# Kernel optimization log

Measured on AMD Instinct MI355X. Metric: run time of the kernel, lower is better.

Reference implementation:

```python
import jax, jax.numpy as jnp
import numpy as np
from functools import partial

INPUT_DIM = 256
HIDDEN = 512
NUM_LAYERS = 2

def _linp(key, fan_in, shape):
    # torch nn.Linear/Conv default init: U(-1/sqrt(fan_in), 1/sqrt(fan_in))
    bound = 1.0 / np.sqrt(fan_in)
    return jax.random.uniform(key, shape, jnp.float32, -bound, bound)

def setup_inputs() -> dict:
    key = jax.random.key(0)
    ks = iter(jax.random.split(key, 64))
    d = {}
    d["x"] = jax.random.normal(next(ks), (32, 16, 1, 64, 64), jnp.float32)
    # encoder convs (OIHW)
    d["conv1_w"] = _linp(next(ks), 1 * 9, (16, 1, 3, 3));   d["conv1_b"] = _linp(next(ks), 1 * 9, (16,))
    d["conv2_w"] = _linp(next(ks), 16 * 9, (32, 16, 3, 3)); d["conv2_b"] = _linp(next(ks), 16 * 9, (32,))
    d["conv3_w"] = _linp(next(ks), 32 * 9, (INPUT_DIM, 32, 3, 3)); d["conv3_b"] = _linp(next(ks), 32 * 9, (INPUT_DIM,))
    # LSTM cells: per layer 4 gate linears (forget, input, cell, output), in = input+hidden
    for j in range(NUM_LAYERS):
        fan = (INPUT_DIM if j == 0 else HIDDEN) + HIDDEN
        for g in ("f", "i", "g", "o"):
            d[f"W{g}{j}"] = _linp(next(ks), fan, (fan, HIDDEN))
            d[f"b{g}{j}"] = _linp(next(ks), fan, (HIDDEN,))
    # classifier
    d["cw1"] = _linp(next(ks), HIDDEN, (HIDDEN, 128)); d["cb1"] = _linp(next(ks), HIDDEN, (128,))
    d["cw2"] = _linp(next(ks), 128, (128, 64));        d["cb2"] = _linp(next(ks), 128, (64,))
    d["cw3"] = _linp(next(ks), 64, (64, 6));           d["cb3"] = _linp(next(ks), 64, (6,))
    return d

def _conv(x, w, b):
    y = jax.lax.conv_general_dilated(x, w, (1, 1), "SAME",
                                     dimension_numbers=("NCHW", "OIHW", "NCHW"))
    return y + b[None, :, None, None]

def _maxpool2(x):
    return jax.lax.reduce_window(x, -jnp.inf, jax.lax.max,
                                 (1, 1, 2, 2), (1, 1, 2, 2), "VALID")

def reference(x, conv1_w, conv1_b, conv2_w, conv2_b, conv3_w, conv3_b,
              Wf0, bf0, Wi0, bi0, Wg0, bg0, Wo0, bo0,
              Wf1, bf1, Wi1, bi1, Wg1, bg1, Wo1, bo1,
              cw1, cb1, cw2, cb2, cw3, cb3):
    B, T, C, H, W = x.shape
    xf = x.reshape(B * T, C, H, W)
    h = _maxpool2(jax.nn.relu(_conv(xf, conv1_w, conv1_b)))
    h = _maxpool2(jax.nn.relu(_conv(h, conv2_w, conv2_b)))
    h = jax.nn.relu(_conv(h, conv3_w, conv3_b))
    emb = h.mean(axis=(2, 3)).reshape(B, T, -1)  # AdaptiveAvgPool2d((1,1)); dropout = identity (eval)

    layers = [(Wf0, bf0, Wi0, bi0, Wg0, bg0, Wo0, bo0),
              (Wf1, bf1, Wi1, bi1, Wg1, bg1, Wo1, bo1)]

    def step(carry, x_t):
        hs, cs = carry
        inp = x_t
        new_h, new_c = [], []
        for j, (Wf, bf, Wi, bi, Wg, bg, Wo, bo) in enumerate(layers):
            comb = jnp.concatenate([inp, hs[j]], axis=1)  # [B, in+H]
            f_t = jax.nn.sigmoid(comb @ Wf + bf)
            i_t = jax.nn.sigmoid(comb @ Wi + bi)
            g_t = jnp.tanh(comb @ Wg + bg)
            o_t = jax.nn.sigmoid(comb @ Wo + bo)
            c_n = f_t * cs[j] + i_t * g_t
            h_n = o_t * jnp.tanh(c_n)
            new_h.append(h_n); new_c.append(c_n)
            inp = h_n
        return (tuple(new_h), tuple(new_c)), None

    h0 = tuple(jnp.zeros((B, HIDDEN), x.dtype) for _ in range(NUM_LAYERS))
    c0 = tuple(jnp.zeros((B, HIDDEN), x.dtype) for _ in range(NUM_LAYERS))
    (hs, _), _ = jax.lax.scan(step, (h0, c0), jnp.swapaxes(emb, 0, 1))
    last = hs[-1]  # [B, HIDDEN], last timestep top-layer h (dropout = identity)

    y = jax.nn.relu(last @ cw1 + cb1)
    y = jax.nn.relu(y @ cw2 + cb2)
    return y @ cw3 + cb3  # [B, 6]
```

## Files before the change

kernel.cpp:

```cpp
#include <hip/hip_runtime.h>
#include <math.h>

__global__ void k_conv1(const float* __restrict__ x, const float* __restrict__ w,
                        const float* __restrict__ bias, float* __restrict__ out) {
  int idx = blockIdx.x * 256 + threadIdx.x;
  int ox = idx & 31, oy = (idx >> 5) & 31, oc = (idx >> 10) & 15, n = idx >> 14;
  const float* im = x + n * 4096;
  float wv[9];
#pragma unroll
  for (int i = 0; i < 9; ++i) wv[i] = w[oc * 9 + i];
  float bs = bias[oc];
  float m = 0.f;
#pragma unroll
  for (int dy = 0; dy < 2; ++dy)
#pragma unroll
    for (int dx = 0; dx < 2; ++dx) {
      int cy = oy * 2 + dy, cx = ox * 2 + dx;
      float s = bs;
#pragma unroll
      for (int ky = 0; ky < 3; ++ky) {
        int yy = cy + ky - 1;
        if (yy < 0 || yy >= 64) continue;
#pragma unroll
        for (int kx = 0; kx < 3; ++kx) {
          int xx = cx + kx - 1;
          if (xx < 0 || xx >= 64) continue;
          s += im[yy * 64 + xx] * wv[ky * 3 + kx];
        }
      }
      m = fmaxf(m, fmaxf(s, 0.f));
    }
  out[idx] = m;
}

__global__ void k_prep_w(const float* __restrict__ w2, float* __restrict__ w2t,
                         const float* __restrict__ w3, float* __restrict__ w3t) {
  int id = blockIdx.x * 256 + threadIdx.x;
  if (id < 73728) {
    int ct = id >> 8, oc = id & 255;
    int c = ct / 9, tap = ct - 9 * c;
    w3t[id] = w3[(oc * 32 + c) * 9 + tap];
  }
  if (id < 4608) {
    int ct = id >> 5, oc = id & 31;
    int c = ct / 9, tap = ct - 9 * c;
    w2t[id] = w2[(oc * 16 + c) * 9 + tap];
  }
}

__global__ __launch_bounds__(256) void k_conv2(
    const float* __restrict__ a1, const float* __restrict__ w2t,
    const float* __restrict__ bias, float* __restrict__ a2) {
  __shared__ __align__(16) float ins[8 * 1024];
  int n = blockIdx.x, ocg = blockIdx.y;
  int tid = threadIdx.x;
  int py = tid >> 4, px = tid & 15;
  int y0 = 2 * py - 1, x0 = 2 * px - 1;
  float acc[16][4] = {};
  const float* wb = w2t + ocg * 16;
  for (int ph = 0; ph < 2; ++ph) {
    __syncthreads();
    const float4* src = (const float4*)(a1 + n * 16384 + ph * 8192);
    for (int i = tid; i < 2048; i += 256) ((float4*)ins)[i] = src[i];
    __syncthreads();
    for (int c = 0; c < 8; ++c) {
      float wv[4][4];
#pragma unroll
      for (int r = 0; r < 4; ++r) {
        int y = y0 + r;
        bool vy = (y >= 0) && (y < 32);
        int yc = vy ? y : 0;
#pragma unroll
        for (int cc = 0; cc < 4; ++cc) {
          int xx = x0 + cc;
          bool vx = (xx >= 0) && (xx < 32);
          int xc = vx ? xx : 0;
          float t = ins[c * 1024 + yc * 32 + xc];
          wv[r][cc] = (vy && vx) ? t : 0.f;
        }
      }
      int ch = ph * 8 + c;
#pragma unroll
      for (int ky = 0; ky < 3; ++ky)
#pragma unroll
        for (int kx = 0; kx < 3; ++kx) {
          const float* w16 = wb + (ch * 9 + ky * 3 + kx) * 32;
#pragma unroll
          for (int i = 0; i < 4; ++i) {
            float vv = wv[(i >> 1) + ky][(i & 1) + kx];
#pragma unroll
            for (int j = 0; j < 16; ++j) acc[j][i] += vv * w16[j];
          }
        }
    }
  }
  const float* bp = bias + ocg * 16;
  float4 o[4];
#pragma unroll
  for (int j = 0; j < 16; ++j) {
    float m = fmaxf(fmaxf(acc[j][0], acc[j][1]), fmaxf(acc[j][2], acc[j][3]));
    ((float*)o)[j] = fmaxf(m + bp[j], 0.f);
  }
  float4* dst = (float4*)(a2 + (size_t)(n * 256 + tid) * 32 + ocg * 16);
#pragma unroll
  for (int q = 0; q < 4; ++q) dst[q] = o[q];
}

__global__ __launch_bounds__(256) void k_conv3(
    const float* __restrict__ a2, const float* __restrict__ w3t,
    const float* __restrict__ bias, float* __restrict__ comb0) {
  __shared__ __align__(16) float ins[324 * 20];
  int n = blockIdx.x, ocb = blockIdx.y;
  int tid = threadIdx.x;
  for (int i = tid; i < 1620; i += 256) ((float4*)ins)[i] = float4{0.f, 0.f, 0.f, 0.f};
  int wvid = __builtin_amdgcn_readfirstlane(tid >> 6);
  int lane = tid & 63;
  int tr = lane >> 4, tc = lane & 15;
  float acc[4][8] = {};
  const float* wbase = w3t + ocb * 32 + wvid * 8;
  const float4* src = (const float4*)(a2 + (size_t)n * 8192);
  for (int hf = 0; hf < 2; ++hf) {
    __syncthreads();
    for (int i = tid; i < 1024; i += 256) {
      int px = i >> 2, cg = i & 3;
      int p = ((px >> 4) + 1) * 18 + (px & 15) + 1;
      ((float4*)ins)[p * 5 + cg] = src[px * 8 + hf * 4 + cg];
    }
    __syncthreads();
    for (int cg = 0; cg < 4; ++cg) {
      float4 v[6][3];
#pragma unroll
      for (int dr = 0; dr < 6; ++dr)
#pragma unroll
        for (int dc = 0; dc < 3; ++dc)
          v[dr][dc] = ((const float4*)ins)[((4 * tr + dr) * 18 + tc + dc) * 5 + cg];
#pragma unroll
      for (int ky = 0; ky < 3; ++ky)
#pragma unroll
        for (int kx = 0; kx < 3; ++kx)
#pragma unroll
          for (int c = 0; c < 4; ++c) {
            const float* w8 = wbase + (((hf * 4 + cg) * 4 + c) * 9 + ky * 3 + kx) * 256;
#pragma unroll
            for (int i = 0; i < 4; ++i) {
              float vv = ((const float*)&v[i + ky][kx])[c];
#pragma unroll
              for (int j = 0; j < 8; ++j) acc[i][j] += vv * w8[j];
            }
          }
    }
  }
  const float* bp = bias + ocb * 32 + wvid * 8;
  int bb = n >> 4, tt = n & 15;
#pragma unroll
  for (int j = 0; j < 8; ++j) {
    float bj = bp[j];
    float s = 0.f;
#pragma unroll
    for (int i = 0; i < 4; ++i) s += fmaxf(acc[i][j] + bj, 0.f);
#pragma unroll
    for (int off = 32; off; off >>= 1) s += __shfl_down(s, off, 64);
    if (lane == 0) {
      int oc = ocb * 32 + wvid * 8 + j;
      comb0[(size_t)(tt * 768 + oc) * 32 + bb] = s * (1.f / 256.f);
    }
  }
}

__global__ void k_pack(const float* __restrict__ Wf, const float* __restrict__ Wi,
                       const float* __restrict__ Wg, const float* __restrict__ Wo,
                       float* __restrict__ p, int fan) {
  __shared__ float t[4][32][33];
  int k0 = blockIdx.x * 32, h0 = blockIdx.y * 32;
  int tx = threadIdx.x & 31, ty = threadIdx.x >> 5;
  const float* Ws[4] = {Wf, Wi, Wg, Wo};
#pragma unroll
  for (int g = 0; g < 4; ++g)
    for (int r = 0; r < 32; r += 8)
      t[g][ty + r][tx] = Ws[g][(size_t)(k0 + ty + r) * 512 + h0 + tx];
  __syncthreads();
  for (int r = 0; r < 32; r += 8) {
    int hh = ty + r;
    float4 v = {t[0][tx][hh], t[1][tx][hh], t[2][tx][hh], t[3][tx][hh]};
    ((float4*)p)[(size_t)(h0 + hh) * fan + k0 + tx] = v;
  }
}

struct SArgs {
  const float* comb;
  const float* pw;
  float* houtA; float* houtB; float* cT;
  const float* bf; const float* bi; const float* bg; const float* bo;
};

template <int FAN>
__device__ __forceinline__ void lstm_sbody(int h, int tid, const SArgs& A,
                                           float* __restrict__ gsum) {
  constexpr int CH = FAN / 8;
  const int wv = __builtin_amdgcn_readfirstlane(tid >> 6);
  const int lane = tid & 63;
  const int ks = lane >> 5, b = lane & 31;
  const int kb = wv * CH;
  const float4* pw4 = (const float4*)A.pw + (size_t)h * FAN + kb;
  const float* ac = A.comb + (size_t)kb * 32 + lane;
  float a0 = 0.f, a1 = 0.f, a2 = 0.f, a3 = 0.f;
#pragma unroll 8
  for (int kk = 0; kk < CH; kk += 2) {
    float4 w0 = pw4[kk];
    float4 w1 = pw4[kk + 1];
    float av = ac[kk * 32];
    a0 += av * (ks ? w1.x : w0.x);
    a1 += av * (ks ? w1.y : w0.y);
    a2 += av * (ks ? w1.z : w0.z);
    a3 += av * (ks ? w1.w : w0.w);
  }
  a0 += __shfl_xor(a0, 32);
  a1 += __shfl_xor(a1, 32);
  a2 += __shfl_xor(a2, 32);
  a3 += __shfl_xor(a3, 32);
  if (lane < 32) {
    gsum[(wv * 4 + 0) * 33 + b] = a0;
    gsum[(wv * 4 + 1) * 33 + b] = a1;
    gsum[(wv * 4 + 2) * 33 + b] = a2;
    gsum[(wv * 4 + 3) * 33 + b] = a3;
  }
  __syncthreads();
  if (tid < 32) {
    float fp = A.bf[h], ip = A.bi[h], gp = A.bg[h], op = A.bo[h];
#pragma unroll
    for (int q = 0; q < 8; ++q) {
      fp += gsum[(q * 4 + 0) * 33 + tid];
      ip += gsum[(q * 4 + 1) * 33 + tid];
      gp += gsum[(q * 4 + 2) * 33 + tid];
      op += gsum[(q * 4 + 3) * 33 + tid];
    }
    float ft = 1.f / (1.f + expf(-fp));
    float it_ = 1.f / (1.f + expf(-ip));
    float gt = tanhf(gp);
    float ot = 1.f / (1.f + expf(-op));
    float cn = ft * A.cT[h * 32 + tid] + it_ * gt;
    A.cT[h * 32 + tid] = cn;
    float hn = ot * tanhf(cn);
    A.houtA[h * 32 + tid] = hn;
    A.houtB[h * 32 + tid] = hn;
  }
}

__global__ __launch_bounds__(512) void k_lstm_s0(SArgs a) {
  __shared__ float gsum[32 * 33];
  lstm_sbody<768>(blockIdx.x, threadIdx.x, a, gsum);
}
__global__ __launch_bounds__(512) void k_lstm_s1(SArgs a) {
  __shared__ float gsum[32 * 33];
  lstm_sbody<1024>(blockIdx.x, threadIdx.x, a, gsum);
}
__global__ __launch_bounds__(512) void k_lstm_spair(SArgs a0, SArgs a1) {
  __shared__ float gsum[32 * 33];
  if (blockIdx.x < 512)
    lstm_sbody<768>(blockIdx.x, threadIdx.x, a0, gsum);
  else
    lstm_sbody<1024>(blockIdx.x - 512, threadIdx.x, a1, gsum);
}

__global__ void k_cls(const float* __restrict__ h1T, const float* __restrict__ cw1,
                      const float* __restrict__ cb1, const float* __restrict__ cw2,
                      const float* __restrict__ cb2, const float* __restrict__ cw3,
                      const float* __restrict__ cb3, float* __restrict__ out) {
  __shared__ float hv[512];
  __shared__ float y1[128];
  __shared__ float y2[64];
  int b = blockIdx.x, tid = threadIdx.x;
  for (int i = tid; i < 512; i += 128) hv[i] = h1T[i * 32 + b];
  __syncthreads();
  float s = cb1[tid];
  for (int k = 0; k < 512; ++k) s += hv[k] * cw1[k * 128 + tid];
  y1[tid] = fmaxf(s, 0.f);
  __syncthreads();
  if (tid < 64) {
    float s2 = cb2[tid];
    for (int k = 0; k < 128; ++k) s2 += y1[k] * cw2[k * 64 + tid];
    y2[tid] = fmaxf(s2, 0.f);
  }
  __syncthreads();
  if (tid < 6) {
    float s3 = cb3[tid];
    for (int k = 0; k < 64; ++k) s3 += y2[k] * cw3[k * 6 + tid];
    out[b * 6 + tid] = s3;
  }
}

extern "C" void kernel_launch(void* const* d_in, const int* in_sizes, int n_in,
                              void* d_out, int out_size, void* d_ws, size_t ws_size,
                              hipStream_t stream) {
  const float* x  = (const float*)d_in[0];
  const float* w1 = (const float*)d_in[1];
  const float* b1 = (const float*)d_in[2];
  const float* w2 = (const float*)d_in[3];
  const float* b2 = (const float*)d_in[4];
  const float* w3 = (const float*)d_in[5];
  const float* b3 = (const float*)d_in[6];
  const float* cw1 = (const float*)d_in[23];
  const float* cb1 = (const float*)d_in[24];
  const float* cw2 = (const float*)d_in[25];
  const float* cb2 = (const float*)d_in[26];
  const float* cw3 = (const float*)d_in[27];
  const float* cb3 = (const float*)d_in[28];

  float* ws = (float*)d_ws;
  float* a1    = ws;
  float* p0    = ws;
  float* p1    = ws + 1572864;
  float* comb0 = ws + 3670016;
  float* comb1 = ws + 4087808;
  float* c0    = ws + 4644864;
  float* c1    = ws + 4661248;
  float* a2    = ws + 8388608;
  float* w2t   = ws + 12582912;
  float* w3t   = ws + 12587520;
  const int C0 = 768 * 32, C1 = 1024 * 32;

  k_prep_w<<<288, 256, 0, stream>>>(w2, w2t, w3, w3t);
  k_conv1<<<32768, 256, 0, stream>>>(x, w1, b1, a1);
  k_conv2<<<dim3(512, 2), 256, 0, stream>>>(a1, w2t, b2, a2);

  hipMemsetAsync(comb0 + 256 * 32, 0, (size_t)512 * 32 * 4, stream);
  hipMemsetAsync(comb1 + 512 * 32, 0, (size_t)512 * 32 * 4, stream);
  hipMemsetAsync(c0, 0, (size_t)2 * 512 * 32 * 4, stream);

  k_conv3<<<dim3(512, 8), 256, 0, stream>>>(a2, w3t, b3, comb0);

  k_pack<<<dim3(24, 16), 256, 0, stream>>>(
      (const float*)d_in[7], (const float*)d_in[9],
      (const float*)d_in[11], (const float*)d_in[13], p0, 768);
  k_pack<<<dim3(32, 16), 256, 0, stream>>>(
      (const float*)d_in[15], (const float*)d_in[17],
      (const float*)d_in[19], (const float*)d_in[21], p1, 1024);

  auto L0 = [&](int t) {
    SArgs a;
    a.comb = comb0 + (size_t)t * C0;
    a.pw = p0;
    a.houtA = comb0 + (size_t)(t + 1) * C0 + 256 * 32;
    a.houtB = comb1 + (size_t)t * C1;
    a.cT = c0;
    a.bf = (const float*)d_in[8];  a.bi = (const float*)d_in[10];
    a.bg = (const float*)d_in[12]; a.bo = (const float*)d_in[14];
    return a;
  };
  auto L1 = [&](int t) {
    SArgs a;
    a.comb = comb1 + (size_t)t * C1;
    a.pw = p1;
    a.houtA = comb1 + (size_t)(t + 1) * C1 + 512 * 32;
    a.houtB = a.houtA;
    a.cT = c1;
    a.bf = (const float*)d_in[16]; a.bi = (const float*)d_in[18];
    a.bg = (const float*)d_in[20]; a.bo = (const float*)d_in[22];
    return a;
  };

  k_lstm_s0<<<512, 512, 0, stream>>>(L0(0));
  for (int p = 0; p < 15; ++p)
    k_lstm_spair<<<1024, 512, 0, stream>>>(L0(p + 1), L1(p));
  k_lstm_s1<<<512, 512, 0, stream>>>(L1(15));

  k_cls<<<32, 128, 0, stream>>>(comb1 + (size_t)16 * C1 + 512 * 32,
                                cw1, cb1, cw2, cb2, cw3, cb3, (float*)d_out);
}
```

Measured before the change: 687.9 us.

## Run LSTM recurrence as one persistent cooperative kernel with grid barrier

Measured after the change: 617.4 us. 10.2% less time.

```diff
diff --git a/kernel.cpp b/kernel.cpp
--- a/kernel.cpp
+++ b/kernel.cpp
@@ -186,9 +186,138 @@
   }
 }
 
+struct Coop2Args {
+  float* comb0; float* comb1;
+  const float* p0; const float* p1;
+  const float* b00; const float* b01; const float* b02; const float* b03;
+  const float* b10; const float* b11; const float* b12; const float* b13;
+  int* bar;
+};
+
+#define COOP2_LDS_BYTES (23040 * 4)
+
+template <int FAN>
+__device__ __forceinline__ void coop_step(
+    int hbase, int tid, const float* __restrict__ comb,
+    const float* __restrict__ wl,
+    float* __restrict__ houtA, float* __restrict__ houtB,
+    float bfv, float biv, float bgv, float bov,
+    float& creg, float* __restrict__ gsum, float* __restrict__ pre) {
+  constexpr int CH = FAN / 32;
+  const int hs = tid >> 8, kc = (tid >> 3) & 31, bq = tid & 7;
+  const float4* w4 = (const float4*)wl + (size_t)hs * FAN + kc * CH;
+  const float4* a4 = (const float4*)comb;
+  const int rot = kc & 7;
+  float4 af{0,0,0,0}, ai{0,0,0,0}, ag{0,0,0,0}, ao{0,0,0,0};
+#pragma unroll
+  for (int kk = 0; kk < CH; ++kk) {
+    int idx = kk + rot; if (idx >= CH) idx -= CH;
+    float4 w = w4[idx];
+    float4 a = a4[(size_t)(kc * CH + idx) * 8 + bq];
+    af.x += w.x*a.x; af.y += w.x*a.y; af.z += w.x*a.z; af.w += w.x*a.w;
+    ai.x += w.y*a.x; ai.y += w.y*a.y; ai.z += w.y*a.z; ai.w += w.y*a.w;
+    ag.x += w.z*a.x; ag.y += w.z*a.y; ag.z += w.z*a.z; ag.w += w.z*a.w;
+    ao.x += w.w*a.x; ao.y += w.w*a.y; ao.z += w.w*a.z; ao.w += w.w*a.w;
+  }
+  __syncthreads();
+  {
+    const float* accs[4] = {(const float*)&af, (const float*)&ai,
+                            (const float*)&ag, (const float*)&ao};
+#pragma unroll
+    for (int g = 0; g < 4; ++g)
+#pragma unroll
+      for (int j = 0; j < 4; ++j)
+        gsum[((hs * 4 + g) * 32 + 4 * bq + j) * 33 + kc] = accs[g][j];
+  }
+  __syncthreads();
+  if (tid < 256) {
+    int hs2 = tid >> 7, g = (tid >> 5) & 3, b = tid & 31;
+    int base = ((hs2 * 4 + g) * 32 + b) * 33;
+    float s = 0.f;
+#pragma unroll
+    for (int q = 0; q < 32; ++q) s += gsum[base + q];
+    pre[(hs2 * 4 + g) * 32 + b] = s;
+  }
+  __syncthreads();
+  if (tid < 64) {
+    int hs2 = tid >> 5, b = tid & 31;
+    float fp = pre[(hs2 * 4 + 0) * 32 + b] + bfv;
+    float ip = pre[(hs2 * 4 + 1) * 32 + b] + biv;
+    float gp = pre[(hs2 * 4 + 2) * 32 + b] + bgv;
+    float op = pre[(hs2 * 4 + 3) * 32 + b] + bov;
+    float ft = 1.f / (1.f + expf(-fp));
+    float it_ = 1.f / (1.f + expf(-ip));
+    float gt = tanhf(gp);
+    float ot = 1.f / (1.f + expf(-op));
+    float cn = ft * creg + it_ * gt;
+    creg = cn;
+    float hn = ot * tanhf(cn);
+    int hh = hbase + hs2;
+    __hip_atomic_store(&houtA[hh * 32 + b], hn, __ATOMIC_RELAXED,
+                       __HIP_MEMORY_SCOPE_AGENT);
+    if (houtB != houtA)
+      __hip_atomic_store(&houtB[hh * 32 + b], hn, __ATOMIC_RELAXED,
+                         __HIP_MEMORY_SCOPE_AGENT);
+  }
+}
+
+__global__ __launch_bounds__(512) void k_lstm_coop2(Coop2Args A) {
+  extern __shared__ float smem[];
+  float* wl0 = smem;
+  float* wl1 = smem + 6144;
+  float* gsum = smem + 14336;
+  float* pre = smem + 22784;
+  const int tid = threadIdx.x;
+  const int hbase = blockIdx.x * 2;
+  for (int i = tid; i < 1536; i += 512) {
+    int hs = i / 768, k = i - hs * 768;
+    ((float4*)wl0)[hs * 768 + k] =
+        ((const float4*)A.p0)[(size_t)(hbase + hs) * 768 + k];
+  }
+  for (int i = tid; i < 2048; i += 512) {
+    int hs = i >> 10, k = i & 1023;
+    ((float4*)wl1)[hs * 1024 + k] =
+        ((const float4*)A.p1)[(size_t)(hbase + hs) * 1024 + k];
+  }
+  float bf0 = 0, bi0 = 0, bg0 = 0, bo0 = 0;
+  float bf1 = 0, bi1 = 0, bg1 = 0, bo1 = 0;
+  if (tid < 64) {
+    int hh = hbase + (tid >> 5);
+    bf0 = A.b00[hh]; bi0 = A.b01[hh]; bg0 = A.b02[hh]; bo0 = A.b03[hh];
+    bf1 = A.b10[hh]; bi1 = A.b11[hh]; bg1 = A.b12[hh]; bo1 = A.b13[hh];
+  }
+  __syncthreads();
+  float c0reg = 0.f, c1reg = 0.f;
+  const int C0 = 768 * 32, C1 = 1024 * 32;
+  for (int it = 0; it <= 16; ++it) {
+    if (it < 16)
+      coop_step<768>(hbase, tid, A.comb0 + (size_t)it * C0, wl0,
+                     A.comb0 + (size_t)(it + 1) * C0 + 256 * 32,
+                     A.comb1 + (size_t)it * C1,
+                     bf0, bi0, bg0, bo0, c0reg, gsum, pre);
+    if (it >= 1)
+      coop_step<1024>(hbase, tid, A.comb1 + (size_t)(it - 1) * C1, wl1,
+                      A.comb1 + (size_t)it * C1 + 512 * 32,
+                      A.comb1 + (size_t)it * C1 + 512 * 32,
+                      bf1, bi1, bg1, bo1, c1reg, gsum, pre);
+    if (it < 16) {
+      __syncthreads();
+      if (tid == 0) {
+        __hip_atomic_fetch_add(A.bar, 1, __ATOMIC_RELEASE,
+                               __HIP_MEMORY_SCOPE_AGENT);
+        const int target = 256 * (it + 1);
+        while (__hip_atomic_load(A.bar, __ATOMIC_RELAXED,
+                                 __HIP_MEMORY_SCOPE_AGENT) < target)
+          __builtin_amdgcn_s_sleep(8);
+        __builtin_amdgcn_fence(__ATOMIC_ACQUIRE, "agent");
+      }
+      __syncthreads();
+    }
+  }
+}
+
 struct SArgs {
-  const float* comb;
-  const float* pw;
+  const float* comb; const float* pw;
   float* houtA; float* houtB; float* cT;
   const float* bf; const float* bi; const float* bg; const float* bo;
 };
@@ -314,6 +443,7 @@
   float* comb1 = ws + 4087808;
   float* c0    = ws + 4644864;
   float* c1    = ws + 4661248;
+  int*   bar   = (int*)(ws + 4677632);
   float* a2    = ws + 8388608;
   float* w2t   = ws + 12582912;
   float* w3t   = ws + 12587520;
@@ -326,6 +456,7 @@
   hipMemsetAsync(comb0 + 256 * 32, 0, (size_t)512 * 32 * 4, stream);
   hipMemsetAsync(comb1 + 512 * 32, 0, (size_t)512 * 32 * 4, stream);
   hipMemsetAsync(c0, 0, (size_t)2 * 512 * 32 * 4, stream);
+  hipMemsetAsync(bar, 0, sizeof(int), stream);
 
   k_conv3<<<dim3(512, 8), 256, 0, stream>>>(a2, w3t, b3, comb0);
 
@@ -336,33 +467,46 @@
       (const float*)d_in[15], (const float*)d_in[17],
       (const float*)d_in[19], (const float*)d_in[21], p1, 1024);
 
-  auto L0 = [&](int t) {
-    SArgs a;
-    a.comb = comb0 + (size_t)t * C0;
-    a.pw = p0;
-    a.houtA = comb0 + (size_t)(t + 1) * C0 + 256 * 32;
-    a.houtB = comb1 + (size_t)t * C1;
-    a.cT = c0;
-    a.bf = (const float*)d_in[8];  a.bi = (const float*)d_in[10];
-    a.bg = (const float*)d_in[12]; a.bo = (const float*)d_in[14];
-    return a;
-  };
-  auto L1 = [&](int t) {
-    SArgs a;
-    a.comb = comb1 + (size_t)t * C1;
-    a.pw = p1;
-    a.houtA = comb1 + (size_t)(t + 1) * C1 + 512 * 32;
-    a.houtB = a.houtA;
-    a.cT = c1;
-    a.bf = (const float*)d_in[16]; a.bi = (const float*)d_in[18];
-    a.bg = (const float*)d_in[20]; a.bo = (const float*)d_in[22];
-    return a;
-  };
-
-  k_lstm_s0<<<512, 512, 0, stream>>>(L0(0));
-  for (int p = 0; p < 15; ++p)
-    k_lstm_spair<<<1024, 512, 0, stream>>>(L0(p + 1), L1(p));
-  k_lstm_s1<<<512, 512, 0, stream>>>(L1(15));
+  Coop2Args ca;
+  ca.comb0 = comb0; ca.comb1 = comb1;
+  ca.p0 = p0; ca.p1 = p1;
+  ca.b00 = (const float*)d_in[8];  ca.b01 = (const float*)d_in[10];
+  ca.b02 = (const float*)d_in[12]; ca.b03 = (const float*)d_in[14];
+  ca.b10 = (const float*)d_in[16]; ca.b11 = (const float*)d_in[18];
+  ca.b12 = (const float*)d_in[20]; ca.b13 = (const float*)d_in[22];
+  ca.bar = bar;
+  void* kargs[] = {&ca};
+  hipError_t cerr = hipLaunchCooperativeKernel(
+      (void*)k_lstm_coop2, dim3(256), dim3(512), kargs, COOP2_LDS_BYTES, stream);
+
+  if (cerr != hipSuccess) {
+    auto L0 = [&](int t) {
+      SArgs a;
+      a.comb = comb0 + (size_t)t * C0;
+      a.pw = p0;
+      a.houtA = comb0 + (size_t)(t + 1) * C0 + 256 * 32;
+      a.houtB = comb1 + (size_t)t * C1;
+      a.cT = c0;
+      a.bf = (const float*)d_in[8];  a.bi = (const float*)d_in[10];
+      a.bg = (const float*)d_in[12]; a.bo = (const float*)d_in[14];
+      return a;
+    };
+    auto L1 = [&](int t) {
+      SArgs a;
+      a.comb = comb1 + (size_t)t * C1;
+      a.pw = p1;
+      a.houtA = comb1 + (size_t)(t + 1) * C1 + 512 * 32;
+      a.houtB = a.houtA;
+      a.cT = c1;
+      a.bf = (const float*)d_in[16]; a.bi = (const float*)d_in[18];
+      a.bg = (const float*)d_in[20]; a.bo = (const float*)d_in[22];
+      return a;
+    };
+    k_lstm_s0<<<512, 512, 0, stream>>>(L0(0));
+    for (int p = 0; p < 15; ++p)
+      k_lstm_spair<<<1024, 512, 0, stream>>>(L0(p + 1), L1(p));
+    k_lstm_s1<<<512, 512, 0, stream>>>(L1(15));
+  }
 
   k_cls<<<32, 128, 0, stream>>>(comb1 + (size_t)16 * C1 + 512 * 32,
                                 cw1, cb1, cw2, cb2, cw3, cb3, (float*)d_out);
```
